# Optimization experiments

Hardware: AMD Instinct MI355X
Metric: run time of the kernel (lower is better)

Reference implementation:

```python
import jax, jax.numpy as jnp
import numpy as np

N_NODES = 50000
N_EDGES = 800000
D_IN = 96
D_EDGE = 32
D_OUT = 96
N_TYPES = 4


def setup_inputs() -> dict:
    key = jax.random.key(0)
    k = jax.random.split(key, 6)
    x = jax.random.normal(k[0], (N_NODES, D_IN), dtype=jnp.float32)
    edge_features = jax.random.normal(k[1], (N_NODES, D_EDGE), dtype=jnp.float32)
    edge_index = jax.random.randint(k[2], (2, N_EDGES), 0, N_NODES, dtype=jnp.int32)
    edge_type = jax.random.randint(k[3], (N_EDGES,), 0, N_TYPES, dtype=jnp.int32)
    # One RelEdgeConv per relation type: Linear(D_IN + D_EDGE -> D_OUT) message fn
    scale = 1.0 / np.sqrt(D_IN + D_EDGE)
    W_msg = jax.random.uniform(k[4], (N_TYPES, D_IN + D_EDGE, D_OUT), jnp.float32, -scale, scale)
    b_msg = jax.random.uniform(k[5], (N_TYPES, D_OUT), jnp.float32, -scale, scale)
    return {"x": x, "edge_features": edge_features, "edge_index": edge_index,
            "edge_type": edge_type, "W_msg": W_msg, "b_msg": b_msg}


def reference(x, edge_features, edge_index, edge_type, W_msg, b_msg):
    # Node-level edge_features (shape[0] == N) -> per-edge relative features
    src, dst = edge_index[0], edge_index[1]
    e = jnp.abs(edge_features[src] - edge_features[dst])          # [E, De]
    feat = jnp.concatenate([x[src], e], axis=-1)                  # [E, Din+De]
    n_nodes = x.shape[0]
    n_types = W_msg.shape[0]

    def per_type(t):
        # relation mask: zero out messages for edges of other types
        mask = (edge_type == t).astype(x.dtype)[:, None]          # [E, 1]
        m = (feat @ W_msg[t] + b_msg[t]) * mask                   # [E, Dout]
        # scatter-add messages to destination nodes
        return jax.ops.segment_sum(m, dst, num_segments=n_nodes)  # [N, Dout]

    out = jnp.stack([per_type(t) for t in range(n_types)])        # [T, N, Dout]
    return out.mean(axis=0)
```

## Files before the change

kernel.cpp:

```cpp
#include <hip/hip_runtime.h>

#define E_EDGES 800000
#define NN 50000
#define D_IN 96
#define D_EDGE 32
#define D_OUT 96
#define KSUM 512
#define SSTRIDE 520
#define NB4 3125
#define BCAP4 384
#define NCHUNK 256
#define CHE 3125
#define CHIT 13
#define BUILD_BLOCKS 512

typedef __attribute__((ext_vector_type(8))) __bf16 bf16x8;
typedef __attribute__((ext_vector_type(4))) float floatx4;

__device__ __forceinline__ float lo16(unsigned int u) {
    return __builtin_bit_cast(float, u << 16);
}
__device__ __forceinline__ float hi16(unsigned int u) {
    return __builtin_bit_cast(float, u & 0xFFFF0000u);
}
__device__ __forceinline__ unsigned int pk2(float a, float b) {
    unsigned short ua = __builtin_bit_cast(unsigned short, (__bf16)a);
    unsigned short ub = __builtin_bit_cast(unsigned short, (__bf16)b);
    return (unsigned int)ua | ((unsigned int)ub << 16);
}

__global__ __launch_bounds__(256) void k_prep(const int* __restrict__ ei,
                                              const int* __restrict__ et,
                                              const float* __restrict__ x,
                                              const float* __restrict__ ef,
                                              const float* __restrict__ Wm,
                                              int* __restrict__ cursor,
                                              int* __restrict__ eb,
                                              __bf16* __restrict__ WT,
                                              unsigned int* __restrict__ xeb) {
    __shared__ int lcnt[NB4];
    __shared__ int gb[NB4];
    int tid = threadIdx.x, bid = blockIdx.x;

    if (bid < NCHUNK) {
        int e0 = bid * CHE;
        for (int i = tid; i < NB4; i += 256) lcnt[i] = 0;
        __syncthreads();

        int pv[CHIT], br[CHIT];
#pragma unroll
        for (int it = 0; it < CHIT; it++) {
            int i = it * 256 + tid;
            br[it] = -1;
            if (i < CHE) {
                int e = e0 + i;
                int dst = ei[E_EDGES + e];
                int b = dst >> 4;
                int rank = atomicAdd(&lcnt[b], 1);
                pv[it] = (ei[e] << 6) | (et[e] << 22) | ((dst & 15) << 24);
                br[it] = rank | (b << 16);
            }
        }
        __syncthreads();
        for (int b = tid; b < NB4; b += 256)
            gb[b] = lcnt[b] ? atomicAdd(&cursor[b], lcnt[b]) : 0;
        __syncthreads();
#pragma unroll
        for (int it = 0; it < CHIT; it++) {
            if (br[it] >= 0) {
                int b = br[it] >> 16, rank = br[it] & 0xFFFF;
                int pos = gb[b] + rank;
                if (pos < BCAP4) eb[b * BCAP4 + pos] = pv[it];
            }
        }
    } else {
        int b2 = bid - NCHUNK;
        int gtid = b2 * 256 + tid;
        int lane = tid & 63, w = tid >> 6;
        for (int n = b2 * 4 + w; n < NN; n += BUILD_BLOCKS * 4) {
            float2 v;
            if (lane < 48) v = *(const float2*)(x  + (size_t)n * D_IN   + 2 * lane);
            else           v = *(const float2*)(ef + (size_t)n * D_EDGE + 2 * (lane - 48));
            xeb[(size_t)n * 64 + lane] = pk2(v.x, v.y);
        }
        for (int i = gtid; i < 96 * KSUM; i += BUILD_BLOCKS * 256) {
            int n = i >> 9, k = i & 511;
            WT[n * KSUM + k] = (__bf16)Wm[(size_t)k * 96 + n];
        }
    }
}

__global__ __launch_bounds__(256) void k_fused(const int* __restrict__ cursor,
                                               const int* __restrict__ eb,
                                               const unsigned int* __restrict__ xeb,
                                               const __bf16* __restrict__ WT,
                                               const float* __restrict__ bm,
                                               float* __restrict__ out) {
    __shared__ int ecopy[BCAP4];
    __shared__ int elist[BCAP4];
    __shared__ int h[64], hbase[64];
    __shared__ int c2[64];
    __shared__ __align__(16) __bf16 Sl[16][SSTRIDE];

    int tid = threadIdx.x, lane = tid & 63, w = tid >> 6;
    int B = blockIdx.x;
    int seg = B * BCAP4;
    int m = min(cursor[B], BCAP4);

    if (tid < 64) h[tid] = 0;
    __syncthreads();

    for (int i = tid; i < m; i += 256) {
        int p = eb[seg + i];
        ecopy[i] = p;
        atomicAdd(&h[(p >> 22) & 63], 1);
    }
    __syncthreads();

    if (w == 0) {
        int v = h[lane];
        int s = v;
        for (int d = 1; d < 64; d <<= 1) {
            int t = __shfl_up(s, d, 64);
            if (lane >= d) s += t;
        }
        hbase[lane] = s - v;
        c2[lane] = s - v;
    }
    __syncthreads();

    for (int i = tid; i < m; i += 256) {
        int p = ecopy[i];
        int pos = atomicAdd(&c2[(p >> 22) & 63], 1);
        elist[pos] = p;
    }
    __syncthreads();

    unsigned int Mmask = (lane >= 48) ? 0x7FFFFFFFu : 0xFFFFFFFFu;
    int quad = lane >> 4, low = lane & 15;

#define EDGE(k) do {                                                           \
        float f0 = lo16(u##k), f1 = hi16(u##k);                                \
        f0 = __builtin_bit_cast(float,                                         \
                 __builtin_bit_cast(unsigned int, f0 - e0) & Mmask);           \
        f1 = __builtin_bit_cast(float,                                         \
                 __builtin_bit_cast(unsigned int, f1 - e1) & Mmask);           \
        sa += (i + k < num) ? f0 : 0.f;                                        \
        sb += (i + k < num) ? f1 : 0.f;                                        \
    } while (0)

    for (int j = 0; j < 4; j++) {
        int nl = w * 4 + j;
        int n = B * 16 + nl;
        float e0 = 0.f, e1 = 0.f;
        if (lane >= 48) {
            unsigned int u = xeb[(size_t)n * 64 + lane];
            e0 = lo16(u); e1 = hi16(u);
        }
        unsigned int* sp = (unsigned int*)&Sl[nl][0];

#pragma unroll
        for (int t = 0; t < 4; t++) {
            int bs = hbase[nl * 4 + t];
            int num = h[nl * 4 + t];
            float sa = 0.f, sb = 0.f;
            for (int i = 0; i < num; i += 4) {
                int i1 = bs + i + 1, i2 = bs + i + 2, i3 = bs + i + 3;
                int lim = m - 1;
                int v0 = elist[bs + i];
                int v1 = elist[i1 < m ? i1 : lim];
                int v2 = elist[i2 < m ? i2 : lim];
                int v3 = elist[i3 < m ? i3 : lim];
                unsigned int u0 = xeb[(v0 & 0x3FFFFF) + lane];
                unsigned int u1 = xeb[(v1 & 0x3FFFFF) + lane];
                unsigned int u2 = xeb[(v2 & 0x3FFFFF) + lane];
                unsigned int u3 = xeb[(v3 & 0x3FFFFF) + lane];
                EDGE(0); EDGE(1); EDGE(2); EDGE(3);
            }
            sp[t * 64 + lane] = pk2(sa, sb);
        }
    }
#undef EDGE
    __syncthreads();

    bf16x8 a[16];
    const __bf16* ap = &Sl[low][0] + quad * 8;
#pragma unroll
    for (int ks = 0; ks < 16; ks++) a[ks] = *(const bf16x8*)(ap + ks * 32);

    for (int ct = w; ct < 6; ct += 4) {
        floatx4 acc = {0.f, 0.f, 0.f, 0.f};
        const __bf16* bp = WT + (size_t)(ct * 16 + low) * KSUM + quad * 8;
#pragma unroll
        for (int ks = 0; ks < 16; ks++)
            acc = __builtin_amdgcn_mfma_f32_16x16x32_bf16(
                a[ks], *(const bf16x8*)(bp + ks * 32), acc, 0, 0, 0);
        int col = ct * 16 + low;
#pragma unroll
        for (int rg = 0; rg < 4; rg++) {
            int r = quad * 4 + rg;
            int g = B * 16 + r;
            float bias = (float)h[r * 4 + 0] * bm[col]
                       + (float)h[r * 4 + 1] * bm[96 + col]
                       + (float)h[r * 4 + 2] * bm[192 + col]
                       + (float)h[r * 4 + 3] * bm[288 + col];
            out[(size_t)g * D_OUT + col] = 0.25f * (acc[rg] + bias);
        }
    }
}

extern "C" void kernel_launch(void* const* d_in, const int* in_sizes, int n_in,
                              void* d_out, int out_size, void* d_ws, size_t ws_size,
                              hipStream_t stream) {
    const float* x  = (const float*)d_in[0];
    const float* ef = (const float*)d_in[1];
    const int*   ei = (const int*)d_in[2];
    const int*   et = (const int*)d_in[3];
    const float* Wm = (const float*)d_in[4];
    const float* bm = (const float*)d_in[5];
    float* out = (float*)d_out;

    int* cursor = (int*)d_ws;
    int* eb     = cursor + 3200;
    __bf16* WT  = (__bf16*)(eb + NB4 * BCAP4);
    unsigned int* xeb = (unsigned int*)(WT + 96 * KSUM);

    hipMemsetAsync(cursor, 0, NB4 * sizeof(int), stream);
    k_prep <<<NCHUNK + BUILD_BLOCKS, 256, 0, stream>>>(ei, et, x, ef, Wm,
                                                       cursor, eb, WT, xeb);
    k_fused<<<NB4, 256, 0, stream>>>(cursor, eb, xeb, WT, bm, out);
}
```

Before: 186.2 us.

## Bucket edges by (node, type) key with global atomics; drop in-kernel sort

Edges are no longer binned per 16-node block and then sorted by (node, type) in shared memory. The prep kernel now scatters each edge's source into a fixed-capacity slot (ECAP=20) for its (dst, type) key, using one global atomic per edge. The fused kernel simply copies that slot array into LDS and skips the histogram, scan and second scatter. The gather loop also handles two types at once to get more loads in flight. The cost is a larger workspace, a larger memset and per-block copy that includes unused padding, heavier global-atomic contention, and edges silently dropped if any (node, type) has more than 20 edges.

After: 211.9 us. +13.8%, slower.

```diff
diff --git a/kernel.cpp b/kernel.cpp
--- a/kernel.cpp
+++ b/kernel.cpp
@@ -8,10 +8,9 @@
 #define KSUM 512
 #define SSTRIDE 520
 #define NB4 3125
-#define BCAP4 384
-#define NCHUNK 256
-#define CHE 3125
-#define CHIT 13
+#define ECAP 20
+#define NKEYS (NB4 * 64)
+#define SCAT_BLOCKS 1024
 #define BUILD_BLOCKS 512
 
 typedef __attribute__((ext_vector_type(8))) __bf16 bf16x8;
@@ -38,43 +37,19 @@
                                               int* __restrict__ eb,
                                               __bf16* __restrict__ WT,
                                               unsigned int* __restrict__ xeb) {
-    __shared__ int lcnt[NB4];
-    __shared__ int gb[NB4];
     int tid = threadIdx.x, bid = blockIdx.x;
 
-    if (bid < NCHUNK) {
-        int e0 = bid * CHE;
-        for (int i = tid; i < NB4; i += 256) lcnt[i] = 0;
-        __syncthreads();
-
-        int pv[CHIT], br[CHIT];
-#pragma unroll
-        for (int it = 0; it < CHIT; it++) {
-            int i = it * 256 + tid;
-            br[it] = -1;
-            if (i < CHE) {
-                int e = e0 + i;
-                int dst = ei[E_EDGES + e];
-                int b = dst >> 4;
-                int rank = atomicAdd(&lcnt[b], 1);
-                pv[it] = (ei[e] << 6) | (et[e] << 22) | ((dst & 15) << 24);
-                br[it] = rank | (b << 16);
-            }
-        }
-        __syncthreads();
-        for (int b = tid; b < NB4; b += 256)
-            gb[b] = lcnt[b] ? atomicAdd(&cursor[b], lcnt[b]) : 0;
-        __syncthreads();
-#pragma unroll
-        for (int it = 0; it < CHIT; it++) {
-            if (br[it] >= 0) {
-                int b = br[it] >> 16, rank = br[it] & 0xFFFF;
-                int pos = gb[b] + rank;
-                if (pos < BCAP4) eb[b * BCAP4 + pos] = pv[it];
-            }
+    if (bid < SCAT_BLOCKS) {
+        for (int e = bid * 256 + tid; e < E_EDGES; e += SCAT_BLOCKS * 256) {
+            int dst = ei[E_EDGES + e];
+            int ty  = et[e];
+            int src = ei[e];
+            int key = ((dst >> 4) << 6) | ((dst & 15) << 2) | ty;
+            int r = atomicAdd(&cursor[key], 1);
+            if (r < ECAP) eb[key * ECAP + r] = src << 6;
         }
     } else {
-        int b2 = bid - NCHUNK;
+        int b2 = bid - SCAT_BLOCKS;
         int gtid = b2 * 256 + tid;
         int lane = tid & 63, w = tid >> 6;
         for (int n = b2 * 4 + w; n < NN; n += BUILD_BLOCKS * 4) {
@@ -96,57 +71,32 @@
                                                const __bf16* __restrict__ WT,
                                                const float* __restrict__ bm,
                                                float* __restrict__ out) {
-    __shared__ int ecopy[BCAP4];
-    __shared__ int elist[BCAP4];
-    __shared__ int h[64], hbase[64];
-    __shared__ int c2[64];
     __shared__ __align__(16) __bf16 Sl[16][SSTRIDE];
+    __shared__ __align__(16) int el[64 * ECAP];
+    __shared__ int h[64];
 
     int tid = threadIdx.x, lane = tid & 63, w = tid >> 6;
     int B = blockIdx.x;
-    int seg = B * BCAP4;
-    int m = min(cursor[B], BCAP4);
 
-    if (tid < 64) h[tid] = 0;
-    __syncthreads();
-
-    for (int i = tid; i < m; i += 256) {
-        int p = eb[seg + i];
-        ecopy[i] = p;
-        atomicAdd(&h[(p >> 22) & 63], 1);
-    }
-    __syncthreads();
-
-    if (w == 0) {
-        int v = h[lane];
-        int s = v;
-        for (int d = 1; d < 64; d <<= 1) {
-            int t = __shfl_up(s, d, 64);
-            if (lane >= d) s += t;
-        }
-        hbase[lane] = s - v;
-        c2[lane] = s - v;
-    }
-    __syncthreads();
-
-    for (int i = tid; i < m; i += 256) {
-        int p = ecopy[i];
-        int pos = atomicAdd(&c2[(p >> 22) & 63], 1);
-        elist[pos] = p;
+    if (tid < 64) h[tid] = min(cursor[B * 64 + tid], ECAP);
+    {
+        const int4* s4 = (const int4*)(eb + (size_t)B * (64 * ECAP));
+        int4* d4 = (int4*)el;
+        for (int i = tid; i < (64 * ECAP) / 4; i += 256) d4[i] = s4[i];
     }
     __syncthreads();
 
     unsigned int Mmask = (lane >= 48) ? 0x7FFFFFFFu : 0xFFFFFFFFu;
     int quad = lane >> 4, low = lane & 15;
 
-#define EDGE(k) do {                                                           \
-        float f0 = lo16(u##k), f1 = hi16(u##k);                                \
+#define EDGE(u, k, nn, sa, sb) do {                                            \
+        float f0 = lo16(u), f1 = hi16(u);                                      \
         f0 = __builtin_bit_cast(float,                                         \
                  __builtin_bit_cast(unsigned int, f0 - e0) & Mmask);           \
         f1 = __builtin_bit_cast(float,                                         \
                  __builtin_bit_cast(unsigned int, f1 - e1) & Mmask);           \
-        sa += (i + k < num) ? f0 : 0.f;                                        \
-        sb += (i + k < num) ? f1 : 0.f;                                        \
+        sa += (i + k < nn) ? f0 : 0.f;                                         \
+        sb += (i + k < nn) ? f1 : 0.f;                                         \
     } while (0)
 
     for (int j = 0; j < 4; j++) {
@@ -160,24 +110,39 @@
         unsigned int* sp = (unsigned int*)&Sl[nl][0];
 
 #pragma unroll
-        for (int t = 0; t < 4; t++) {
-            int bs = hbase[nl * 4 + t];
-            int num = h[nl * 4 + t];
-            float sa = 0.f, sb = 0.f;
-            for (int i = 0; i < num; i += 4) {
-                int i1 = bs + i + 1, i2 = bs + i + 2, i3 = bs + i + 3;
-                int lim = m - 1;
-                int v0 = elist[bs + i];
-                int v1 = elist[i1 < m ? i1 : lim];
-                int v2 = elist[i2 < m ? i2 : lim];
-                int v3 = elist[i3 < m ? i3 : lim];
-                unsigned int u0 = xeb[(v0 & 0x3FFFFF) + lane];
-                unsigned int u1 = xeb[(v1 & 0x3FFFFF) + lane];
-                unsigned int u2 = xeb[(v2 & 0x3FFFFF) + lane];
-                unsigned int u3 = xeb[(v3 & 0x3FFFFF) + lane];
-                EDGE(0); EDGE(1); EDGE(2); EDGE(3);
+        for (int tp = 0; tp < 2; tp++) {
+            int k0 = nl * 4 + 2 * tp;
+            int n0 = h[k0], n1 = h[k0 + 1];
+            const int* q0 = el + k0 * ECAP;
+            const int* q1 = q0 + ECAP;
+            float sa0 = 0.f, sb0 = 0.f, sa1 = 0.f, sb1 = 0.f;
+            int mx = max(n0, n1);
+            for (int i = 0; i < mx; i += 4) {
+                unsigned int u0=0,u1=0,u2=0,u3=0, v0=0,v1=0,v2=0,v3=0;
+                bool on0 = i < n0, on1 = i < n1;
+                if (on0) {
+                    int4 a = *(const int4*)(q0 + i);
+                    int a1 = (i + 1 < n0) ? a.y : a.x;
+                    int a2 = (i + 2 < n0) ? a.z : a.x;
+                    int a3 = (i + 3 < n0) ? a.w : a.x;
+                    u0 = xeb[a.x + lane]; u1 = xeb[a1 + lane];
+                    u2 = xeb[a2 + lane]; u3 = xeb[a3 + lane];
+                }
+                if (on1) {
+                    int4 b = *(const int4*)(q1 + i);
+                    int b1 = (i + 1 < n1) ? b.y : b.x;
+                    int b2 = (i + 2 < n1) ? b.z : b.x;
+                    int b3 = (i + 3 < n1) ? b.w : b.x;
+                    v0 = xeb[b.x + lane]; v1 = xeb[b1 + lane];
+                    v2 = xeb[b2 + lane]; v3 = xeb[b3 + lane];
+                }
+                if (on0) { EDGE(u0,0,n0,sa0,sb0); EDGE(u1,1,n0,sa0,sb0);
+                           EDGE(u2,2,n0,sa0,sb0); EDGE(u3,3,n0,sa0,sb0); }
+                if (on1) { EDGE(v0,0,n1,sa1,sb1); EDGE(v1,1,n1,sa1,sb1);
+                           EDGE(v2,2,n1,sa1,sb1); EDGE(v3,3,n1,sa1,sb1); }
             }
-            sp[t * 64 + lane] = pk2(sa, sb);
+            sp[(2 * tp) * 64 + lane]     = pk2(sa0, sb0);
+            sp[(2 * tp + 1) * 64 + lane] = pk2(sa1, sb1);
         }
     }
 #undef EDGE
@@ -221,12 +186,12 @@
     float* out = (float*)d_out;
 
     int* cursor = (int*)d_ws;
-    int* eb     = cursor + 3200;
-    __bf16* WT  = (__bf16*)(eb + NB4 * BCAP4);
+    int* eb     = cursor + NKEYS;
+    __bf16* WT  = (__bf16*)(eb + NKEYS * ECAP);
     unsigned int* xeb = (unsigned int*)(WT + 96 * KSUM);
 
-    hipMemsetAsync(cursor, 0, NB4 * sizeof(int), stream);
-    k_prep <<<NCHUNK + BUILD_BLOCKS, 256, 0, stream>>>(ei, et, x, ef, Wm,
-                                                       cursor, eb, WT, xeb);
+    hipMemsetAsync(cursor, 0, NKEYS * sizeof(int), stream);
+    k_prep <<<SCAT_BLOCKS + BUILD_BLOCKS, 256, 0, stream>>>(ei, et, x, ef, Wm,
+                                                            cursor, eb, WT, xeb);
     k_fused<<<NB4, 256, 0, stream>>>(cursor, eb, xeb, WT, bm, out);
 }
```
